# Performance work log

Hardware: AMD Instinct MI355X
Metric: run time of the kernel (lower is better)

Reference implementation:

```python
import jax, jax.numpy as jnp
import numpy as np

B_CHUNK = 5          # hardcoded self.B in the module
GAMMA = 0.9865
BATCH, SEQ, FEAT, DIM = 8, 4000, 256, 256


def setup_inputs() -> dict:
    key = jax.random.key(0)
    ks = jax.random.split(key, 6)
    xq = jax.random.normal(ks[0], (BATCH, SEQ, FEAT), jnp.float32)
    xk = jax.random.normal(ks[1], (BATCH, SEQ, FEAT), jnp.float32)
    xv = jax.random.normal(ks[2], (BATCH, SEQ, FEAT), jnp.float32)
    scale = 1.0 / np.sqrt(FEAT).astype(np.float32)
    Wq = jax.random.normal(ks[3], (FEAT, DIM), jnp.float32) * scale
    Wk = jax.random.normal(ks[4], (FEAT, DIM), jnp.float32) * scale
    Wv = jax.random.normal(ks[5], (FEAT, DIM), jnp.float32) * scale
    return {"xq": xq, "xk": xk, "xv": xv, "Wq": Wq, "Wk": Wk, "Wv": Wv}


def reference(xq, xk, xv, Wq, Wk, Wv):
    gamma = jnp.float32(GAMMA)
    B = B_CHUNK
    b, seq, _ = xq.shape
    dim = Wq.shape[1]
    n = seq // B  # number of chunks

    # projections, chunked: [b, n, B, dim]
    Q = (xq @ Wq).reshape(b, n, B, dim)
    K = (xk @ Wk).reshape(b, n, B, dim)
    V = (xv @ Wv).reshape(b, n, B, dim)

    chunk_idx = jnp.arange(n, dtype=jnp.float32)
    # Z[i] = gamma^(B - i - 1) (per-chunk scalar, as in original)
    Z = gamma ** (jnp.float32(B) - chunk_idx - 1.0)
    Vz = V * Z[None, :, None, None]

    # intra-chunk decay matrix: L[i,j] = gamma^(j-i) for i >= j, else 0
    pos = jnp.arange(B, dtype=jnp.float32)
    L = jnp.tril(gamma ** (pos[None, :] - pos[:, None]))

    # intra-chunk term: (Q K^T * L) @ V, vectorized over all chunks
    S = jnp.einsum('bnid,bnjd->bnij', Q, K)          # [b, n, B, B]
    intra = jnp.einsum('bnij,bnjd->bnid', S * L, V)  # [b, n, B, dim]

    # cross-chunk recurrence: R[i] = K_i^T Vz_i + gamma^B R[i-1]
    # X[i-1] += Q_i @ R[i-1] * gamma^(i+1)
    Qn = jnp.moveaxis(Q, 1, 0)   # [n, b, B, dim]
    Kn = jnp.moveaxis(K, 1, 0)
    Vzn = jnp.moveaxis(Vz, 1, 0)
    gB = gamma ** B

    def step(R_prev, inp):
        qi, ki, vzi, i = inp
        cross_prev = jnp.einsum('bod,bde->boe', qi, R_prev) * gamma ** (i + 1.0)
        R_new = jnp.einsum('bod,boe->bde', ki, vzi) + gB * R_prev
        return R_new, cross_prev

    R0 = jnp.zeros((b, dim, dim), xq.dtype)
    _, ys = jax.lax.scan(step, R0, (Qn, Kn, Vzn, chunk_idx))  # ys[i] = cross for chunk i-1
    cross = jnp.concatenate([ys[1:], jnp.zeros_like(ys[:1])], axis=0)  # last chunk has no cross term
    cross = jnp.moveaxis(cross, 0, 1)  # [b, n, B, dim]

    X = intra + cross
    return X.reshape(b, seq, dim)
```

## Files before the change

kernel.cpp:

```cpp
#include <hip/hip_runtime.h>
#include <cmath>

#define GAMMA 0.9865f
#define L2G   -0.01960905f
#define BATCH 8
#define SEQ   4000
#define CSUP  25
#define GSUP  32
#define RPG   125

typedef _Float16 half8 __attribute__((ext_vector_type(8)));
typedef _Float16 half4 __attribute__((ext_vector_type(4)));
typedef float    floatx4 __attribute__((ext_vector_type(4)));

__device__ __forceinline__ float gpow(float e) { return exp2f(e * L2G); }

__global__ __launch_bounds__(256) void wt_convert(
    const float* __restrict__ Wq, const float* __restrict__ Wk, const float* __restrict__ Wv,
    _Float16* __restrict__ Wt) {
    int t = blockIdx.x * 256 + threadIdx.x;
    int mat = t >> 16, rem = t & 65535;
    int n = rem >> 8, k = rem & 255;
    const float* W = (mat == 0) ? Wq : (mat == 1) ? Wk : Wv;
    Wt[(size_t)mat * 65536 + n * 256 + k] = (_Float16)W[k * 256 + n];
}

__global__ __launch_bounds__(256, 2) void qkv_gemm_f16(
    const float* __restrict__ xq, const float* __restrict__ xk, const float* __restrict__ xv,
    const _Float16* __restrict__ WtAll,
    _Float16* __restrict__ Qb, _Float16* __restrict__ Kb, _Float16* __restrict__ Vb) {
    int op = blockIdx.y;
    const float* x = (op == 0) ? xq : (op == 1) ? xk : xv;
    const _Float16* Wt = WtAll + (size_t)op * 65536;
    _Float16* dst = (op == 0) ? Qb : (op == 1) ? Kb : Vb;

    __shared__ _Float16 Xs[128][40];
    __shared__ _Float16 WsT[256][40];

    int t = threadIdx.x;
    int lane = t & 63, wave = t >> 6;
    int ln = lane & 15, q8 = (lane >> 4) << 3, q4 = (lane >> 4) << 2;
    int row0 = blockIdx.x * 128;

    floatx4 acc[8][4] = {};

    for (int dt = 0; dt < 8; ++dt) {
        int k0 = dt * 32;
#pragma unroll
        for (int i = 0; i < 4; ++i) {
            int idx = t + i * 256;
            int m = idx >> 3, kk = (idx & 7) << 2;
            floatx4 v = *(const floatx4*)&x[(size_t)(row0 + m) * 256 + k0 + kk];
            half4 h; h[0] = (_Float16)v[0]; h[1] = (_Float16)v[1];
            h[2] = (_Float16)v[2]; h[3] = (_Float16)v[3];
            *(half4*)&Xs[m][kk] = h;
        }
#pragma unroll
        for (int i = 0; i < 4; ++i) {
            int idx = t + i * 256;
            int n = idx >> 2, kk = (idx & 3) << 3;
            *(half8*)&WsT[n][kk] = *(const half8*)&Wt[n * 256 + k0 + kk];
        }
        __syncthreads();
        half8 af[8];
#pragma unroll
        for (int mi = 0; mi < 8; ++mi) af[mi] = *(const half8*)&Xs[mi * 16 + ln][q8];
#pragma unroll
        for (int ni = 0; ni < 4; ++ni) {
            half8 bf = *(const half8*)&WsT[(wave * 4 + ni) * 16 + ln][q8];
#pragma unroll
            for (int mi = 0; mi < 8; ++mi)
                acc[mi][ni] = __builtin_amdgcn_mfma_f32_16x16x32_f16(af[mi], bf, acc[mi][ni], 0, 0, 0);
        }
        __syncthreads();
    }
#pragma unroll
    for (int mi = 0; mi < 8; ++mi)
#pragma unroll
        for (int ni = 0; ni < 4; ++ni)
#pragma unroll
            for (int r = 0; r < 4; ++r) {
                int row = row0 + mi * 16 + q4 + r;
                int col = (wave * 4 + ni) * 16 + ln;
                dst[(size_t)row * 256 + col] = (_Float16)acc[mi][ni][r];
            }
}

__global__ __launch_bounds__(256, 2) void chunk_states_mfma(
    const _Float16* __restrict__ Kb, const _Float16* __restrict__ Vb,
    _Float16* __restrict__ Wh) {
    int eh = blockIdx.x, g = blockIdx.y, b = blockIdx.z;
    int t = threadIdx.x, lane = t & 63, wave = t >> 6;
    int ln = lane & 15, q8 = (lane >> 4) << 3, q4 = (lane >> 4) << 2;
    __shared__ __align__(16) _Float16 Vs[32 * 136];
    __shared__ __align__(16) _Float16 Ks[32 * 264];
    size_t base_row = (size_t)b * SEQ + g * RPG;
    floatx4 acc[8][4] = {};
    for (int kt = 0; kt < 4; ++kt) {
        int r0 = kt * 32;
#pragma unroll
        for (int i = 0; i < 2; ++i) {
            int idx = t + i * 256;
            int r = idx >> 4, e8 = (idx & 15) << 3;
            half8 v = {};
            if (r0 + r < RPG) {
                v = *(const half8*)&Vb[(base_row + r0 + r) * 256 + eh * 128 + e8];
                int mloc = (r0 + r) / 5;
                float a = gpow((float)(149 - 6 * mloc));
#pragma unroll
                for (int z = 0; z < 8; ++z) v[z] = (_Float16)((float)v[z] * a);
            }
            *(half8*)&Vs[r * 136 + e8] = v;
        }
#pragma unroll
        for (int i = 0; i < 4; ++i) {
            int idx = t + i * 256;
            int r = idx >> 5, d8 = (idx & 31) << 3;
            half8 v = {};
            if (r0 + r < RPG) v = *(const half8*)&Kb[(base_row + r0 + r) * 256 + d8];
            *(half8*)&Ks[r * 264 + d8] = v;
        }
        __syncthreads();
        half8 Af[8], Bf[4];
#pragma unroll
        for (int mi = 0; mi < 8; ++mi)
#pragma unroll
            for (int j = 0; j < 8; ++j) Af[mi][j] = Vs[(q8 + j) * 136 + mi * 16 + ln];
#pragma unroll
        for (int ni = 0; ni < 4; ++ni)
#pragma unroll
            for (int j = 0; j < 8; ++j) Bf[ni][j] = Ks[(q8 + j) * 264 + wave * 64 + ni * 16 + ln];
#pragma unroll
        for (int mi = 0; mi < 8; ++mi)
#pragma unroll
            for (int ni = 0; ni < 4; ++ni)
                acc[mi][ni] = __builtin_amdgcn_mfma_f32_16x16x32_f16(Af[mi], Bf[ni], acc[mi][ni], 0, 0, 0);
        __syncthreads();
    }
    size_t ob = ((size_t)(g * 8 + b)) << 16;
#pragma unroll
    for (int mi = 0; mi < 8; ++mi)
#pragma unroll
        for (int ni = 0; ni < 4; ++ni)
#pragma unroll
            for (int r = 0; r < 4; ++r) {
                int e = eh * 128 + mi * 16 + q4 + r;
                int d = wave * 64 + ni * 16 + ln;
                Wh[ob + (size_t)e * 256 + d] = (_Float16)acc[mi][ni][r];
            }
}

__global__ __launch_bounds__(256) void state_scan(
    const _Float16* __restrict__ Wh, _Float16* __restrict__ SprevT) {
    int t = blockIdx.x * 256 + threadIdx.x;
    int b = t >> 13;
    int idx = (t & 8191) << 3;
    const float gF = gpow(150.0f);
    float s[8] = {};
    for (int g = 0; g < GSUP; ++g) {
        size_t o = (((size_t)(g * 8 + b)) << 16) + idx;
        half8 w = *(const half8*)&Wh[o];
        half8 sv;
#pragma unroll
        for (int z = 0; z < 8; ++z) { sv[z] = (_Float16)s[z]; s[z] = (float)w[z] + gF * s[z]; }
        *(half8*)&SprevT[o] = sv;
    }
}

__global__ __launch_bounds__(256) void intra_sc(
    const _Float16* __restrict__ Qb, const _Float16* __restrict__ Kb, float* __restrict__ scw) {
    int b = blockIdx.y;
    int j = blockIdx.x * 4 + (threadIdx.x >> 6);
    int lane = threadIdx.x & 63;
    size_t base = ((size_t)b * SEQ + j * 5) * 256 + lane * 4;
    half4 qv[5], kv[5];
#pragma unroll
    for (int p = 0; p < 5; ++p) {
        qv[p] = *(const half4*)&Qb[base + p * 256];
        kv[p] = *(const half4*)&Kb[base + p * 256];
    }
#pragma unroll
    for (int p = 0; p < 5; ++p)
#pragma unroll
        for (int q = 0; q <= p; ++q) {
            float s = 0.f;
#pragma unroll
            for (int z = 0; z < 4; ++z) s += (float)qv[p][z] * (float)kv[q][z];
#pragma unroll
            for (int off = 32; off; off >>= 1) s += __shfl_xor(s, off, 64);
            if (lane == 0) scw[((size_t)b * 800 + j) * 25 + p * 5 + q] = s * gpow((float)(q - p));
        }
}

__global__ __launch_bounds__(256, 2) void cross_f16(
    const _Float16* __restrict__ Qb, const _Float16* __restrict__ Kb,
    const _Float16* __restrict__ Vb, const _Float16* __restrict__ SprevT,
    const float* __restrict__ scw, float* __restrict__ out) {
    int eq = blockIdx.x, g = blockIdx.y, b = blockIdx.z;
    int e0 = eq * 64;
    int t = threadIdx.x;
    int lane = t & 63, wave = t >> 6;
    int ln = lane & 15, q8 = (lane >> 4) << 3, q4 = (lane >> 4) << 2;
    int m4 = (wave >> 1) * 4;
    int c4 = (wave & 1) * 4;
    int e2 = (wave & 1) * 2;

    __shared__ __align__(16) char smem[60416];
    _Float16* QsB  = (_Float16*)smem;
    _Float16* KsB  = (_Float16*)(smem + 10240);
    _Float16* VsTB = (_Float16*)smem;
    _Float16* SsB  = (_Float16*)(smem + 20480);
    _Float16* PsB  = (_Float16*)(smem + 25600);
#define QS(m_, k_)  QsB[(m_) * 40 + (k_)]
#define KS(m_, k_)  KsB[(m_) * 40 + (k_)]
#define SS(m_, k_)  SsB[(m_) * 40 + (k_)]
#define PS(m_, k_)  PsB[(m_) * 136 + (k_)]
#define VST(m_, k_) VsTB[(m_) * 136 + (k_)]

    size_t kvbase = (size_t)b * SEQ + g * RPG;
    size_t sb = ((size_t)(g * 8 + b)) << 16;

    floatx4 pacc[4][4] = {};
    floatx4 acc[4][2] = {};

    for (int dt = 0; dt < 8; ++dt) {
        int d0 = dt * 32;
#pragma unroll
        for (int i = 0; i < 2; ++i) {
            int idx = t + i * 256;
            int m = idx >> 2, kk = (idx & 3) << 3;
            int qr = g * RPG + 5 + m;
            half8 v = {};
            if (m < 125 && qr < SEQ) v = *(const half8*)&Qb[((size_t)b * SEQ + qr) * 256 + d0 + kk];
            *(half8*)&QS(m, kk) = v;
        }
#pragma unroll
        for (int i = 0; i < 2; ++i) {
            int idx = t + i * 256;
            int cp = idx >> 2, kk = (idx & 3) << 3;
            half8 v = {};
            if (cp < 125) v = *(const half8*)&Kb[(kvbase + cp) * 256 + d0 + kk];
            *(half8*)&KS(cp, kk) = v;
        }
        {
            int ee = t >> 2, kk = (t & 3) << 3;
            *(half8*)&SS(ee, kk) = *(const half8*)&SprevT[sb + (size_t)(e0 + ee) * 256 + d0 + kk];
        }
        __syncthreads();
        half8 af[4];
#pragma unroll
        for (int mi = 0; mi < 4; ++mi) af[mi] = *(const half8*)&QS((m4 + mi) * 16 + ln, q8);
#pragma unroll
        for (int ci = 0; ci < 4; ++ci) {
            half8 bf = *(const half8*)&KS((c4 + ci) * 16 + ln, q8);
#pragma unroll
            for (int mi = 0; mi < 4; ++mi)
                pacc[mi][ci] = __builtin_amdgcn_mfma_f32_16x16x32_f16(af[mi], bf, pacc[mi][ci], 0, 0, 0);
        }
#pragma unroll
        for (int ei = 0; ei < 2; ++ei) {
            half8 bf = *(const half8*)&SS((e2 + ei) * 16 + ln, q8);
#pragma unroll
            for (int mi = 0; mi < 4; ++mi)
                acc[mi][ei] = __builtin_amdgcn_mfma_f32_16x16x32_f16(af[mi], bf, acc[mi][ei], 0, 0, 0);
        }
        __syncthreads();
    }

#pragma unroll
    for (int mi = 0; mi < 4; ++mi)
#pragma unroll
        for (int r = 0; r < 4; ++r) {
            int rp = (m4 + mi) * 16 + q4 + r;
            int rc = rp / 5;
            float rs = 0.f;
            if (rp < 125 && !(g == GSUP - 1 && rc == CSUP - 1)) rs = gpow((float)(6 * rc + 7));
            acc[mi][0][r] *= rs;
            acc[mi][1][r] *= rs;
        }

#pragma unroll
    for (int i = 0; i < 32; ++i) {
        int idx = t + i * 256;
        int cp = idx >> 6, ee = idx & 63;
        _Float16 v = (_Float16)0.f;
        if (cp < 125) v = Vb[(kvbase + cp) * 256 + e0 + ee];
        VST(ee, cp) = v;
    }
#pragma unroll
    for (int mi = 0; mi < 4; ++mi)
#pragma unroll
        for (int ci = 0; ci < 4; ++ci)
#pragma unroll
            for (int r = 0; r < 4; ++r) {
                int rp = (m4 + mi) * 16 + q4 + r;
                int cp = (c4 + ci) * 16 + ln;
                int rc = rp / 5, cc = cp / 5;
                float w = 0.f;
                if (rp < 125 && cp < 125 && cc <= rc && !(g == GSUP - 1 && rc == CSUP - 1))
                    w = gpow((float)(6 * (rc - cc + 1)));
                PS(rp, cp) = (_Float16)(pacc[mi][ci][r] * w);
            }
    __syncthreads();

#pragma unroll
    for (int ct = 0; ct < 4; ++ct) {
        int cp0 = ct * 32;
        half8 paf[4];
#pragma unroll
        for (int mi = 0; mi < 4; ++mi) paf[mi] = *(const half8*)&PS((m4 + mi) * 16 + ln, cp0 + q8);
#pragma unroll
        for (int ei = 0; ei < 2; ++ei) {
            half8 bv = *(const half8*)&VST((e2 + ei) * 16 + ln, cp0 + q8);
#pragma unroll
            for (int mi = 0; mi < 4; ++mi)
                acc[mi][ei] = __builtin_amdgcn_mfma_f32_16x16x32_f16(paf[mi], bv, acc[mi][ei], 0, 0, 0);
        }
    }

#pragma unroll
    for (int mi = 0; mi < 4; ++mi)
#pragma unroll
        for (int r = 0; r < 4; ++r) {
            int rp = (m4 + mi) * 16 + q4 + r;
            if (rp < 125) {
                int rc = rp / 5, pp = rp - rc * 5;
                const float* srow = scw + ((size_t)b * 800 + g * 25 + rc) * 25 + pp * 5;
                float a0 = acc[mi][0][r], a1 = acc[mi][1][r];
                for (int q = 0; q <= pp; ++q) {
                    float s = srow[q];
                    a0 += s * (float)VST(e2 * 16 + ln, rc * 5 + q);
                    a1 += s * (float)VST((e2 + 1) * 16 + ln, rc * 5 + q);
                }
                size_t orow = ((size_t)b * SEQ + g * RPG + rp) * 256;
                out[orow + e0 + e2 * 16 + ln] = a0;
                out[orow + e0 + (e2 + 1) * 16 + ln] = a1;
            }
        }
}

extern "C" void kernel_launch(void* const* d_in, const int* in_sizes, int n_in,
                              void* d_out, int out_size, void* d_ws, size_t ws_size,
                              hipStream_t stream) {
    const float* xq = (const float*)d_in[0];
    const float* xk = (const float*)d_in[1];
    const float* xv = (const float*)d_in[2];
    const float* Wq = (const float*)d_in[3];
    const float* Wk = (const float*)d_in[4];
    const float* Wv = (const float*)d_in[5];
    float* out = (float*)d_out;

    const size_t NELEM = (size_t)SEQ * BATCH * 256;
    _Float16* Qb = (_Float16*)d_ws;
    _Float16* Kb = Qb + NELEM;
    _Float16* Vb = Kb + NELEM;
    _Float16* Wt = Vb + NELEM;
    _Float16* Wh = Wt + 196608;
    _Float16* SprevT = Wh + (size_t)GSUP * BATCH * 65536;
    float* scw = (float*)(SprevT + (size_t)GSUP * BATCH * 65536);

    wt_convert<<<dim3(768), 256, 0, stream>>>(Wq, Wk, Wv, Wt);
    qkv_gemm_f16<<<dim3(250, 3), 256, 0, stream>>>(xq, xk, xv, Wt, Qb, Kb, Vb);
    chunk_states_mfma<<<dim3(2, 32, 8), 256, 0, stream>>>(Kb, Vb, Wh);
    state_scan<<<dim3(256), 256, 0, stream>>>(Wh, SprevT);
    intra_sc<<<dim3(200, 8), 256, 0, stream>>>(Qb, Kb, scw);
    cross_f16<<<dim3(4, 32, 8), 256, 0, stream>>>(Qb, Kb, Vb, SprevT, scw, out);
}
```

Measured before the change: 275.1 us.

## Load cross-kernel MFMA operands directly from global memory and use odd-stride LDS padding

The cross kernel now reads Q, K and the previous-state operands straight from global memory into MFMA registers instead of staging them in shared memory each d-tile. This removes the per-iteration barriers. V is transposed into LDS once up front, the decay factors come from small shared tables, and the launch bound asks for 3 blocks per CU. Separately, chunk_states and the cross kernel switch to odd LDS strides with scalar stores and loads, and state_scan uses half4 per thread with twice as many blocks. The risks are uncoalesced global fragment loads and many scalar LDS accesses in place of vector ones.

```diff
diff --git a/kernel.cpp b/kernel.cpp
--- a/kernel.cpp
+++ b/kernel.cpp
@@ -92,8 +92,8 @@
     int eh = blockIdx.x, g = blockIdx.y, b = blockIdx.z;
     int t = threadIdx.x, lane = t & 63, wave = t >> 6;
     int ln = lane & 15, q8 = (lane >> 4) << 3, q4 = (lane >> 4) << 2;
-    __shared__ __align__(16) _Float16 Vs[32 * 136];
-    __shared__ __align__(16) _Float16 Ks[32 * 264];
+    __shared__ _Float16 Vs[32 * 137];
+    __shared__ _Float16 Ks[32 * 265];
     size_t base_row = (size_t)b * SEQ + g * RPG;
     floatx4 acc[8][4] = {};
     for (int kt = 0; kt < 4; ++kt) {
@@ -110,7 +110,8 @@
 #pragma unroll
                 for (int z = 0; z < 8; ++z) v[z] = (_Float16)((float)v[z] * a);
             }
-            *(half8*)&Vs[r * 136 + e8] = v;
+#pragma unroll
+            for (int z = 0; z < 8; ++z) Vs[r * 137 + e8 + z] = v[z];
         }
 #pragma unroll
         for (int i = 0; i < 4; ++i) {
@@ -118,18 +119,19 @@
             int r = idx >> 5, d8 = (idx & 31) << 3;
             half8 v = {};
             if (r0 + r < RPG) v = *(const half8*)&Kb[(base_row + r0 + r) * 256 + d8];
-            *(half8*)&Ks[r * 264 + d8] = v;
+#pragma unroll
+            for (int z = 0; z < 8; ++z) Ks[r * 265 + d8 + z] = v[z];
         }
         __syncthreads();
         half8 Af[8], Bf[4];
 #pragma unroll
         for (int mi = 0; mi < 8; ++mi)
 #pragma unroll
-            for (int j = 0; j < 8; ++j) Af[mi][j] = Vs[(q8 + j) * 136 + mi * 16 + ln];
+            for (int j = 0; j < 8; ++j) Af[mi][j] = Vs[(q8 + j) * 137 + mi * 16 + ln];
 #pragma unroll
         for (int ni = 0; ni < 4; ++ni)
 #pragma unroll
-            for (int j = 0; j < 8; ++j) Bf[ni][j] = Ks[(q8 + j) * 264 + wave * 64 + ni * 16 + ln];
+            for (int j = 0; j < 8; ++j) Bf[ni][j] = Ks[(q8 + j) * 265 + wave * 64 + ni * 16 + ln];
 #pragma unroll
         for (int mi = 0; mi < 8; ++mi)
 #pragma unroll
@@ -153,17 +155,17 @@
 __global__ __launch_bounds__(256) void state_scan(
     const _Float16* __restrict__ Wh, _Float16* __restrict__ SprevT) {
     int t = blockIdx.x * 256 + threadIdx.x;
-    int b = t >> 13;
-    int idx = (t & 8191) << 3;
+    int b = t >> 14;
+    int idx = (t & 16383) << 2;
     const float gF = gpow(150.0f);
-    float s[8] = {};
+    float s[4] = {};
     for (int g = 0; g < GSUP; ++g) {
         size_t o = (((size_t)(g * 8 + b)) << 16) + idx;
-        half8 w = *(const half8*)&Wh[o];
-        half8 sv;
-#pragma unroll
-        for (int z = 0; z < 8; ++z) { sv[z] = (_Float16)s[z]; s[z] = (float)w[z] + gF * s[z]; }
-        *(half8*)&SprevT[o] = sv;
+        half4 w = *(const half4*)&Wh[o];
+        half4 sv;
+#pragma unroll
+        for (int z = 0; z < 4; ++z) { sv[z] = (_Float16)s[z]; s[z] = (float)w[z] + gF * s[z]; }
+        *(half4*)&SprevT[o] = sv;
     }
 }
 
@@ -192,7 +194,7 @@
         }
 }
 
-__global__ __launch_bounds__(256, 2) void cross_f16(
+__global__ __launch_bounds__(256, 3) void cross_f16(
     const _Float16* __restrict__ Qb, const _Float16* __restrict__ Kb,
     const _Float16* __restrict__ Vb, const _Float16* __restrict__ SprevT,
     const float* __restrict__ scw, float* __restrict__ out) {
@@ -205,67 +207,60 @@
     int c4 = (wave & 1) * 4;
     int e2 = (wave & 1) * 2;
 
-    __shared__ __align__(16) char smem[60416];
-    _Float16* QsB  = (_Float16*)smem;
-    _Float16* KsB  = (_Float16*)(smem + 10240);
-    _Float16* VsTB = (_Float16*)smem;
-    _Float16* SsB  = (_Float16*)(smem + 20480);
-    _Float16* PsB  = (_Float16*)(smem + 25600);
-#define QS(m_, k_)  QsB[(m_) * 40 + (k_)]
-#define KS(m_, k_)  KsB[(m_) * 40 + (k_)]
-#define SS(m_, k_)  SsB[(m_) * 40 + (k_)]
-#define PS(m_, k_)  PsB[(m_) * 136 + (k_)]
-#define VST(m_, k_) VsTB[(m_) * 136 + (k_)]
+    __shared__ float rtab[25];
+    __shared__ float gtabm[25];
+    __shared__ _Float16 PsB[128 * 130];
+    __shared__ _Float16 VsB[64 * 130];
+
+    if (t < 25) { rtab[t] = gpow((float)(6 * t + 7)); gtabm[t] = gpow((float)(6 * (t + 1))); }
 
     size_t kvbase = (size_t)b * SEQ + g * RPG;
     size_t sb = ((size_t)(g * 8 + b)) << 16;
+    size_t qrow0 = (size_t)b * SEQ;
+
+#pragma unroll
+    for (int i = 0; i < 4; ++i) {
+        int idx = t + i * 256;
+        int cp = idx >> 3, e8 = (idx & 7) << 3;
+        half8 v = {};
+        if (cp < 125) v = *(const half8*)&Vb[(kvbase + cp) * 256 + e0 + e8];
+#pragma unroll
+        for (int z = 0; z < 8; ++z) VsB[(e8 + z) * 130 + cp] = v[z];
+    }
 
     floatx4 pacc[4][4] = {};
     floatx4 acc[4][2] = {};
 
     for (int dt = 0; dt < 8; ++dt) {
         int d0 = dt * 32;
-#pragma unroll
-        for (int i = 0; i < 2; ++i) {
-            int idx = t + i * 256;
-            int m = idx >> 2, kk = (idx & 3) << 3;
-            int qr = g * RPG + 5 + m;
+        half8 af[4];
+#pragma unroll
+        for (int mi = 0; mi < 4; ++mi) {
+            int rp = (m4 + mi) * 16 + ln;
+            int qr = g * RPG + 5 + rp;
             half8 v = {};
-            if (m < 125 && qr < SEQ) v = *(const half8*)&Qb[((size_t)b * SEQ + qr) * 256 + d0 + kk];
-            *(half8*)&QS(m, kk) = v;
-        }
-#pragma unroll
-        for (int i = 0; i < 2; ++i) {
-            int idx = t + i * 256;
-            int cp = idx >> 2, kk = (idx & 3) << 3;
-            half8 v = {};
-            if (cp < 125) v = *(const half8*)&Kb[(kvbase + cp) * 256 + d0 + kk];
-            *(half8*)&KS(cp, kk) = v;
-        }
-        {
-            int ee = t >> 2, kk = (t & 3) << 3;
-            *(half8*)&SS(ee, kk) = *(const half8*)&SprevT[sb + (size_t)(e0 + ee) * 256 + d0 + kk];
-        }
-        __syncthreads();
-        half8 af[4];
-#pragma unroll
-        for (int mi = 0; mi < 4; ++mi) af[mi] = *(const half8*)&QS((m4 + mi) * 16 + ln, q8);
+            if (rp < 125 && qr < SEQ) v = *(const half8*)&Qb[(qrow0 + qr) * 256 + d0 + q8];
+            af[mi] = v;
+        }
 #pragma unroll
         for (int ci = 0; ci < 4; ++ci) {
-            half8 bf = *(const half8*)&KS((c4 + ci) * 16 + ln, q8);
+            int cp = (c4 + ci) * 16 + ln;
+            half8 bf = {};
+            if (cp < 125) bf = *(const half8*)&Kb[(kvbase + cp) * 256 + d0 + q8];
 #pragma unroll
             for (int mi = 0; mi < 4; ++mi)
                 pacc[mi][ci] = __builtin_amdgcn_mfma_f32_16x16x32_f16(af[mi], bf, pacc[mi][ci], 0, 0, 0);
         }
 #pragma unroll
         for (int ei = 0; ei < 2; ++ei) {
-            half8 bf = *(const half8*)&SS((e2 + ei) * 16 + ln, q8);
+            half8 bf = *(const half8*)&SprevT[sb + (size_t)(e0 + (e2 + ei) * 16 + ln) * 256 + d0 + q8];
 #pragma unroll
             for (int mi = 0; mi < 4; ++mi)
                 acc[mi][ei] = __builtin_amdgcn_mfma_f32_16x16x32_f16(af[mi], bf, acc[mi][ei], 0, 0, 0);
         }
-        __syncthreads();
-    }
+    }
+
+    __syncthreads();
 
 #pragma unroll
     for (int mi = 0; mi < 4; ++mi)
@@ -274,19 +269,11 @@
             int rp = (m4 + mi) * 16 + q4 + r;
             int rc = rp / 5;
             float rs = 0.f;
-            if (rp < 125 && !(g == GSUP - 1 && rc == CSUP - 1)) rs = gpow((float)(6 * rc + 7));
+            if (rp < 125 && !(g == GSUP - 1 && rc == CSUP - 1)) rs = rtab[rc];
             acc[mi][0][r] *= rs;
             acc[mi][1][r] *= rs;
         }
 
-#pragma unroll
-    for (int i = 0; i < 32; ++i) {
-        int idx = t + i * 256;
-        int cp = idx >> 6, ee = idx & 63;
-        _Float16 v = (_Float16)0.f;
-        if (cp < 125) v = Vb[(kvbase + cp) * 256 + e0 + ee];
-        VST(ee, cp) = v;
-    }
 #pragma unroll
     for (int mi = 0; mi < 4; ++mi)
 #pragma unroll
@@ -298,8 +285,8 @@
                 int rc = rp / 5, cc = cp / 5;
                 float w = 0.f;
                 if (rp < 125 && cp < 125 && cc <= rc && !(g == GSUP - 1 && rc == CSUP - 1))
-                    w = gpow((float)(6 * (rc - cc + 1)));
-                PS(rp, cp) = (_Float16)(pacc[mi][ci][r] * w);
+                    w = gtabm[rc - cc];
+                PsB[rp * 130 + cp] = (_Float16)(pacc[mi][ci][r] * w);
             }
     __syncthreads();
 
@@ -308,10 +295,16 @@
         int cp0 = ct * 32;
         half8 paf[4];
 #pragma unroll
-        for (int mi = 0; mi < 4; ++mi) paf[mi] = *(const half8*)&PS((m4 + mi) * 16 + ln, cp0 + q8);
+        for (int mi = 0; mi < 4; ++mi)
+#pragma unroll
+            for (int j = 0; j < 8; ++j)
+                paf[mi][j] = PsB[((m4 + mi) * 16 + ln) * 130 + cp0 + q8 + j];
 #pragma unroll
         for (int ei = 0; ei < 2; ++ei) {
-            half8 bv = *(const half8*)&VST((e2 + ei) * 16 + ln, cp0 + q8);
+            half8 bv;
+#pragma unroll
+            for (int j = 0; j < 8; ++j)
+                bv[j] = VsB[((e2 + ei) * 16 + ln) * 130 + cp0 + q8 + j];
 #pragma unroll
             for (int mi = 0; mi < 4; ++mi)
                 acc[mi][ei] = __builtin_amdgcn_mfma_f32_16x16x32_f16(paf[mi], bv, acc[mi][ei], 0, 0, 0);
@@ -329,8 +322,8 @@
                 float a0 = acc[mi][0][r], a1 = acc[mi][1][r];
                 for (int q = 0; q <= pp; ++q) {
                     float s = srow[q];
-                    a0 += s * (float)VST(e2 * 16 + ln, rc * 5 + q);
-                    a1 += s * (float)VST((e2 + 1) * 16 + ln, rc * 5 + q);
+                    a0 += s * (float)VsB[(e2 * 16 + ln) * 130 + rc * 5 + q];
+                    a1 += s * (float)VsB[((e2 + 1) * 16 + ln) * 130 + rc * 5 + q];
                 }
                 size_t orow = ((size_t)b * SEQ + g * RPG + rp) * 256;
                 out[orow + e0 + e2 * 16 + ln] = a0;
@@ -362,7 +355,7 @@
     wt_convert<<<dim3(768), 256, 0, stream>>>(Wq, Wk, Wv, Wt);
     qkv_gemm_f16<<<dim3(250, 3), 256, 0, stream>>>(xq, xk, xv, Wt, Qb, Kb, Vb);
     chunk_states_mfma<<<dim3(2, 32, 8), 256, 0, stream>>>(Kb, Vb, Wh);
-    state_scan<<<dim3(256), 256, 0, stream>>>(Wh, SprevT);
+    state_scan<<<dim3(512), 256, 0, stream>>>(Wh, SprevT);
     intra_sc<<<dim3(200, 8), 256, 0, stream>>>(Qb, Kb, scw);
     cross_f16<<<dim3(4, 32, 8), 256, 0, stream>>>(Qb, Kb, Vb, SprevT, scw, out);
 }
```

Measured after the change: 290.5 us. +5.6%, slower.
